# Performance work log

Measured on AMD Instinct MI355X. Metric: run time of the kernel, lower is better.

Reference implementation:

```python
import jax, jax.numpy as jnp
import numpy as np

H, O, E, V = 128, 128, 512, 34
B, T, L = 64, 2048, 256


def _lstm(x, wih, whh, bih, bhh):
    # x: [T, B, Din] -> outputs [T, B, H]; PyTorch gate order i, f, g, o
    n = whh.shape[1]
    h0 = jnp.zeros((x.shape[1], n), x.dtype)
    b = bih + bhh
    def step(carry, xt):
        h, c = carry
        g = xt @ wih.T + h @ whh.T + b
        i, f, gg, o = jnp.split(g, 4, axis=-1)
        c = jax.nn.sigmoid(f) * c + jax.nn.sigmoid(i) * jnp.tanh(gg)
        h = jax.nn.sigmoid(o) * jnp.tanh(c)
        return (h, c), h
    _, ys = jax.lax.scan(step, (h0, h0), x)
    return ys


def _conv1d_s2(x, w, b):
    # x: [B, Cin, T], w: [Cout, Cin, 2], kernel=2 stride=2 valid
    y = jax.lax.conv_general_dilated(x, w, (2,), 'VALID', dimension_numbers=('NCH', 'OIH', 'NCH'))
    return y + b[None, :, None]


def setup_inputs():
    key = jax.random.key(0)
    ctr = [0]
    def mk(shape, s=0.05):
        ctr[0] += 1
        return jax.random.normal(jax.random.fold_in(key, ctr[0]), shape, dtype=jnp.float32) * s
    inp = {}
    inp['utter'] = mk((B, T, 40), 1.0)
    inp['targets'] = jax.random.randint(jax.random.fold_in(key, 999), (B, L), 0, V)
    inp['wih_f'] = mk((4 * H, 40)); inp['whh_f'] = mk((4 * H, H)); inp['bih_f'] = mk((4 * H,)); inp['bhh_f'] = mk((4 * H,))
    inp['wih_r'] = mk((4 * H, 40)); inp['whh_r'] = mk((4 * H, H)); inp['bih_r'] = mk((4 * H,)); inp['bhh_r'] = mk((4 * H,))
    inp['c1w'] = mk((H, 2 * H, 2)); inp['c1b'] = mk((H,))
    inp['wih1'] = mk((4 * H, H)); inp['whh1'] = mk((4 * H, H)); inp['bih1'] = mk((4 * H,)); inp['bhh1'] = mk((4 * H,))
    inp['c2w'] = mk((H, H, 2)); inp['c2b'] = mk((H,))
    inp['wih2'] = mk((4 * H, H)); inp['whh2'] = mk((4 * H, H)); inp['bih2'] = mk((4 * H,)); inp['bhh2'] = mk((4 * H,))
    inp['kw'] = mk((O, H)); inp['kb'] = mk((O,)); inp['vw'] = mk((O, H)); inp['vb'] = mk((O,))
    inp['wihd'] = mk((4 * O, O + E)); inp['whhd'] = mk((4 * O, O)); inp['bihd'] = mk((4 * O,)); inp['bhhd'] = mk((4 * O,))
    inp['w1'] = mk((V, O)); inp['b1'] = mk((V,)); inp['w2'] = mk((V, O)); inp['b2'] = mk((V,))
    inp['w3'] = mk((V, V)); inp['b3'] = mk((V,))
    inp['emb'] = mk((V, E), 1.0)
    inp['sh0'] = mk((B, O)); inp['sc0'] = mk((B, O))
    return inp


def _forward(utter, targets, wih_f, whh_f, bih_f, bhh_f, wih_r, whh_r, bih_r, bhh_r,
             c1w, c1b, wih1, whh1, bih1, bhh1, c2w, c2b, wih2, whh2, bih2, bhh2,
             kw, kb, vw, vb, wihd, whhd, bihd, bhhd, w1, b1, w2, b2, w3, b3,
             emb, sh0, sc0):
    # ---- Listener (encoder) ----
    x = jnp.transpose(utter, (1, 0, 2))            # [T, B, 40]
    fwd = _lstm(x, wih_f, whh_f, bih_f, bhh_f)
    bwd = _lstm(x[::-1], wih_r, whh_r, bih_r, bhh_r)[::-1]
    h = jnp.concatenate([fwd, bwd], axis=-1)       # [T, B, 2H]
    h = jnp.transpose(h, (1, 2, 0))                # [B, 2H, T]
    h = _conv1d_s2(h, c1w, c1b)                    # [B, H, T/2]
    h = jnp.transpose(h, (2, 0, 1))                # [T/2, B, H]
    h = _lstm(h, wih1, whh1, bih1, bhh1)
    h = jnp.transpose(h, (1, 2, 0))
    h = _conv1d_s2(h, c2w, c2b)                    # [B, H, T/4]
    h = jnp.transpose(h, (2, 0, 1))
    h = _lstm(h, wih2, whh2, bih2, bhh2)
    h = jnp.transpose(h, (1, 0, 2))                # [B, T/4, H]
    hk = h @ kw.T + kb                              # [B, T/4, O]
    hv = h @ vw.T + vb
    # ---- Speller (decoder) ----
    ys = jnp.transpose(emb[targets], (1, 0, 2))[:-1]   # [L-1, B, E]
    mask = jnp.ones((utter.shape[0], hk.shape[1]), utter.dtype)  # all full-length
    bd = bihd + bhhd
    def step(carry, y_in):
        c, sh, sc = carry
        g = jnp.concatenate([y_in, c], axis=1) @ wihd.T + sh @ whhd.T + bd
        i, f, gg, o = jnp.split(g, 4, axis=-1)
        sc_n = jax.nn.sigmoid(f) * sc + jax.nn.sigmoid(i) * jnp.tanh(gg)
        sh_n = jax.nn.sigmoid(o) * jnp.tanh(sc_n)
        # NOTE: original attends with the cell state sc (faithful to source)
        att = jax.nn.softmax(jnp.einsum('btd,bd->bt', hk, sc_n), axis=1) * mask
        att = att / jnp.sum(att, axis=1, keepdims=True)
        c_n = jnp.einsum('bt,btd->bd', att, hv)
        out = jax.nn.relu(sh_n @ w1.T + b1 + c_n @ w2.T + b2)
        out = jax.nn.softmax(out @ w3.T + b3, axis=1)
        return (c_n, sh_n, sc_n), out
    c0 = jnp.zeros_like(sh0)
    _, preds = jax.lax.scan(step, (c0, sh0, sc0), ys)
    return jnp.transpose(preds, (1, 0, 2))         # [B, L-1, V]


def reference(utter, targets, wih_f, whh_f, bih_f, bhh_f, wih_r, whh_r, bih_r, bhh_r,
              c1w, c1b, wih1, whh1, bih1, bhh1, c2w, c2b, wih2, whh2, bih2, bhh2,
              kw, kb, vw, vb, wihd, whhd, bihd, bhhd, w1, b1, w2, b2, w3, b3,
              emb, sh0, sc0):
    return _forward(utter, targets, wih_f, whh_f, bih_f, bhh_f, wih_r, whh_r, bih_r, bhh_r,
                    c1w, c1b, wih1, whh1, bih1, bhh1, c2w, c2b, wih2, whh2, bih2, bhh2,
                    kw, kb, vw, vb, wihd, whhd, bihd, bhhd, w1, b1, w2, b2, w3, b3,
                    emb, sh0, sc0)
```

## Files before the change

### kernel.cpp

```cpp
#include <hip/hip_runtime.h>

typedef _Float16 half_t;
typedef _Float16 __attribute__((ext_vector_type(2))) half2_t;

__device__ __forceinline__ float fdot2_(half2_t a, half2_t b, float c) {
#if __has_builtin(__builtin_amdgcn_fdot2)
    return __builtin_amdgcn_fdot2(a, b, c, false);
#else
    return c + (float)a[0] * (float)b[0] + (float)a[1] * (float)b[1];
#endif
}
__device__ __forceinline__ half2_t h2(float a, float b) {
    half2_t r; r[0] = (half_t)a; r[1] = (half_t)b; return r;
}
__device__ __forceinline__ half2_t bc2(unsigned int u) {
    return __builtin_bit_cast(half2_t, u);
}
__device__ __forceinline__ unsigned int pk2(float a, float b) {
    return __builtin_bit_cast(unsigned int, h2(a, b));
}
__device__ __forceinline__ float sigm(float x) { return 1.0f / (1.0f + __expf(-x)); }
__device__ __forceinline__ float tanh_(float x) { return 1.0f - 2.0f / (1.0f + __expf(2.0f * x)); }
__device__ __forceinline__ unsigned int packbf2(float a, float b) {
    unsigned int ua = __float_as_uint(a);
    ua = (ua + 0x7fffu + ((ua >> 16) & 1u)) >> 16;
    unsigned int ub = __float_as_uint(b);
    ub = (ub + 0x7fffu + ((ub >> 16) & 1u)) >> 16;
    return ua | (ub << 16);
}
__device__ __forceinline__ float blo(unsigned int u) { return __uint_as_float(u << 16); }
__device__ __forceinline__ float bhi(unsigned int u) { return __uint_as_float(u & 0xffff0000u); }

#define ATTRS1024 __attribute__((amdgpu_flat_work_group_size(1024, 1024)))

__global__ __launch_bounds__(512, 1) void lstm1_k(
    const float* __restrict__ utter,
    const float* __restrict__ wih_f, const float* __restrict__ whh_f,
    const float* __restrict__ bih_f, const float* __restrict__ bhh_f,
    const float* __restrict__ wih_r, const float* __restrict__ whh_r,
    const float* __restrict__ bih_r, const float* __restrict__ bhh_r,
    unsigned short* __restrict__ Hf, unsigned short* __restrict__ Hr)
{
    const int tid = threadIdx.x;
    const int b   = blockIdx.x & 63;
    const int dir = blockIdx.x >> 6;
    const float* wih = dir ? wih_r : wih_f;
    const float* whh = dir ? whh_r : whh_f;
    const float* bih = dir ? bih_r : bih_f;
    const float* bhh = dir ? bhh_r : bhh_f;
    unsigned short* Hout = dir ? Hr : Hf;

    __shared__ float gates[512];
    __shared__ __align__(16) half_t h_h[128];
    __shared__ __align__(16) half_t x2[3][48];

    const int j = tid;
    unsigned int wr2[64];
    {
        const float4* wp = reinterpret_cast<const float4*>(whh + j * 128);
#pragma unroll
        for (int m = 0; m < 32; ++m) {
            float4 v = wp[m];
            wr2[2 * m]     = pk2(v.x, v.y);
            wr2[2 * m + 1] = pk2(v.z, v.w);
        }
    }
    unsigned int wx2[20];
    {
        const float4* xp = reinterpret_cast<const float4*>(wih + j * 40);
#pragma unroll
        for (int q = 0; q < 10; ++q) {
            float4 v = xp[q];
            wx2[2 * q]     = pk2(v.x, v.y);
            wx2[2 * q + 1] = pk2(v.z, v.w);
        }
    }
    const float bias = bih[j] + bhh[j];
    float c = 0.0f;
    if (tid < 128) h_h[tid] = (half_t)0.0f;
    if (tid < 40) {
        int tt0 = dir ? 2047 : 0;
        x2[0][tid] = (half_t)utter[((size_t)b * 2048 + tt0) * 40 + tid];
    } else if (tid < 80) {
        int tt1 = dir ? 2046 : 1;
        x2[1][tid - 40] = (half_t)utter[((size_t)b * 2048 + tt1) * 40 + (tid - 40)];
    }
    __syncthreads();

    for (int t = 0; t < 2048; ++t) {
        const int cur = t % 3;
        const int nx2 = (t + 2) % 3;
        float xn = 0.0f;
        const int tq = tid - 128;
        if (tq >= 0 && tq < 40) {
            int tn = (t + 2 < 2048) ? (t + 2) : 2047;
            int ttn = dir ? (2047 - tn) : tn;
            xn = utter[((size_t)b * 2048 + ttn) * 40 + tq];
        }
        float g0 = bias, g1 = 0.f, g2 = 0.f, g3 = 0.f;
        {
            const uint4* x4p = reinterpret_cast<const uint4*>(&x2[cur][0]);
#pragma unroll
            for (int q = 0; q < 5; ++q) {
                uint4 u = x4p[q];
                g0 = fdot2_(bc2(wx2[4 * q]),     bc2(u.x), g0);
                g1 = fdot2_(bc2(wx2[4 * q + 1]), bc2(u.y), g1);
                g2 = fdot2_(bc2(wx2[4 * q + 2]), bc2(u.z), g2);
                g3 = fdot2_(bc2(wx2[4 * q + 3]), bc2(u.w), g3);
            }
            const uint4* h4p = reinterpret_cast<const uint4*>(h_h);
#pragma unroll
            for (int q = 0; q < 16; ++q) {
                uint4 u = h4p[q];
                g0 = fdot2_(bc2(wr2[4 * q]),     bc2(u.x), g0);
                g1 = fdot2_(bc2(wr2[4 * q + 1]), bc2(u.y), g1);
                g2 = fdot2_(bc2(wr2[4 * q + 2]), bc2(u.z), g2);
                g3 = fdot2_(bc2(wr2[4 * q + 3]), bc2(u.w), g3);
            }
        }
        gates[j] = (g0 + g1) + (g2 + g3);
        __syncthreads();
        if (tid < 128) {
            float i_ = sigm(gates[tid]);
            float f_ = sigm(gates[128 + tid]);
            float g_ = tanh_(gates[256 + tid]);
            float o_ = sigm(gates[384 + tid]);
            c = f_ * c + i_ * g_;
            float hh = o_ * tanh_(c);
            half_t hx = (half_t)hh;
            h_h[tid] = hx;
            int tt = dir ? (2047 - t) : t;
            Hout[((size_t)tt * 64 + b) * 128 + tid] = __builtin_bit_cast(unsigned short, hx);
        } else if (tq < 40) {
            x2[nx2][tq] = (half_t)xn;
        }
        __syncthreads();
    }
}

__global__ __launch_bounds__(512, 1) void lstm_k(
    const unsigned short* __restrict__ Ph,
    const float* __restrict__ whh,
    void* __restrict__ Hout, int T, int outHalf)
{
    const int tid = threadIdx.x;
    const int b = blockIdx.x;
    const int j = tid;
    __shared__ float gates[512];
    __shared__ __align__(16) half_t h_h[128];
    unsigned int wr2[64];
    {
        const float4* wp = reinterpret_cast<const float4*>(whh + j * 128);
#pragma unroll
        for (int m = 0; m < 32; ++m) {
            float4 v = wp[m];
            wr2[2 * m]     = pk2(v.x, v.y);
            wr2[2 * m + 1] = pk2(v.z, v.w);
        }
    }
    float c = 0.0f;
    if (tid < 128) h_h[tid] = (half_t)0.0f;
    const size_t pbase = (size_t)b * T;
    float p_cur = (float)__builtin_bit_cast(half_t, Ph[(pbase + 0) * 512 + j]);
    float p_n1  = (float)__builtin_bit_cast(half_t, Ph[(pbase + 1) * 512 + j]);
    __syncthreads();
    for (int t = 0; t < T; ++t) {
        int tn = (t + 2 < T) ? (t + 2) : (T - 1);
        float p_n2 = (float)__builtin_bit_cast(half_t, Ph[(pbase + tn) * 512 + j]);
        float g0 = p_cur, g1 = 0.f, g2 = 0.f, g3 = 0.f;
        const uint4* h4p = reinterpret_cast<const uint4*>(h_h);
#pragma unroll
        for (int q = 0; q < 16; ++q) {
            uint4 u = h4p[q];
            g0 = fdot2_(bc2(wr2[4 * q]),     bc2(u.x), g0);
            g1 = fdot2_(bc2(wr2[4 * q + 1]), bc2(u.y), g1);
            g2 = fdot2_(bc2(wr2[4 * q + 2]), bc2(u.z), g2);
            g3 = fdot2_(bc2(wr2[4 * q + 3]), bc2(u.w), g3);
        }
        gates[j] = (g0 + g1) + (g2 + g3);
        __syncthreads();
        if (tid < 128) {
            float i_ = sigm(gates[tid]);
            float f_ = sigm(gates[128 + tid]);
            float g_ = tanh_(gates[256 + tid]);
            float o_ = sigm(gates[384 + tid]);
            c = f_ * c + i_ * g_;
            float hh = o_ * tanh_(c);
            half_t hx = (half_t)hh;
            h_h[tid] = hx;
            size_t oi = ((size_t)t * 64 + b) * 128 + tid;
            if (outHalf) ((unsigned short*)Hout)[oi] = __builtin_bit_cast(unsigned short, hx);
            else         ((float*)Hout)[oi] = hh;
        }
        __syncthreads();
        p_cur = p_n1;
        p_n1 = p_n2;
    }
}

template <int CIN>
__global__ __launch_bounds__(128) void conv_k(
    const unsigned short* __restrict__ HA, const unsigned short* __restrict__ HB,
    const float* __restrict__ W, const float* __restrict__ bias,
    float* __restrict__ out, int Tout)
{
    __shared__ __align__(16) float xin[64 * CIN];
    const int b = blockIdx.x;
    const int t0 = blockIdx.y * 32;
    const int tid = threadIdx.x;
    for (int idx = tid; idx < 64 * CIN; idx += 128) {
        int tl = idx / CIN, ci = idx % CIN;
        int tau = t0 * 2 + tl;
        unsigned short u;
        if constexpr (CIN == 256) {
            u = (ci < 128) ? HA[(size_t)tau * 8192 + b * 128 + ci]
                           : HB[(size_t)tau * 8192 + b * 128 + (ci - 128)];
        } else {
            u = HA[(size_t)tau * 8192 + b * 128 + ci];
        }
        xin[idx] = (float)__builtin_bit_cast(half_t, u);
    }
    __syncthreads();
    const int co = tid;
    float acc[32];
#pragma unroll
    for (int u = 0; u < 32; ++u) acc[u] = 0.0f;
    const float4* Wrow4 = reinterpret_cast<const float4*>(W + (size_t)co * 2 * CIN);
    const float4* xin4 = reinterpret_cast<const float4*>(xin);
    for (int c4 = 0; c4 < CIN / 4; ++c4) {
        float4 wA = Wrow4[2 * c4];
        float4 wB = Wrow4[2 * c4 + 1];
#pragma unroll
        for (int u = 0; u < 32; ++u) {
            float4 x0 = xin4[(2 * u) * (CIN / 4) + c4];
            float4 x1 = xin4[(2 * u + 1) * (CIN / 4) + c4];
            acc[u] += wA.x * x0.x + wA.y * x1.x + wA.z * x0.y + wA.w * x1.y
                    + wB.x * x0.z + wB.y * x1.z + wB.z * x0.w + wB.w * x1.w;
        }
    }
    float bs = bias[co];
#pragma unroll
    for (int u = 0; u < 32; ++u)
        out[((size_t)b * Tout + t0 + u) * 128 + co] = acc[u] + bs;
}

__global__ __launch_bounds__(256) void gemm_k(
    const float* __restrict__ A, const float* __restrict__ W, int ldw,
    const float* __restrict__ bias1, const float* __restrict__ bias2,
    void* __restrict__ C, int M, int N, int K, int mode, int Tdim)
{
    __shared__ __align__(16) float As[16][68];
    __shared__ __align__(16) float Ws[16][68];
    const int tid = threadIdx.x;
    const int m0 = blockIdx.x * 64, n0 = blockIdx.y * 64;
    const int kk = tid & 15, mm = tid >> 4;
    const int tm = tid & 15, tn = tid >> 4;
    float acc[4][4];
#pragma unroll
    for (int i = 0; i < 4; ++i)
#pragma unroll
        for (int jj = 0; jj < 4; ++jj) acc[i][jj] = 0.0f;

    for (int k0 = 0; k0 < K; k0 += 16) {
#pragma unroll
        for (int r = 0; r < 4; ++r) {
            As[kk][mm + 16 * r] = A[(size_t)(m0 + mm + 16 * r) * K + k0 + kk];
            Ws[kk][mm + 16 * r] = W[(size_t)(n0 + mm + 16 * r) * ldw + k0 + kk];
        }
        __syncthreads();
#pragma unroll
        for (int q = 0; q < 16; ++q) {
            float4 a = reinterpret_cast<const float4*>(&As[q][0])[tm];
            float4 w = reinterpret_cast<const float4*>(&Ws[q][0])[tn];
            acc[0][0] += a.x * w.x; acc[0][1] += a.x * w.y; acc[0][2] += a.x * w.z; acc[0][3] += a.x * w.w;
            acc[1][0] += a.y * w.x; acc[1][1] += a.y * w.y; acc[1][2] += a.y * w.z; acc[1][3] += a.y * w.w;
            acc[2][0] += a.z * w.x; acc[2][1] += a.z * w.y; acc[2][2] += a.z * w.z; acc[2][3] += a.z * w.w;
            acc[3][0] += a.w * w.x; acc[3][1] += a.w * w.y; acc[3][2] += a.w * w.z; acc[3][3] += a.w * w.w;
        }
        __syncthreads();
    }
    float bv[4];
#pragma unroll
    for (int jj = 0; jj < 4; ++jj) {
        int n = n0 + tn * 4 + jj;
        float v = 0.0f;
        if (bias1) v += bias1[n];
        if (bias2) v += bias2[n];
        bv[jj] = v;
    }
#pragma unroll
    for (int i = 0; i < 4; ++i) {
        int m = m0 + tm * 4 + i;
#pragma unroll
        for (int jj = 0; jj < 4; ++jj) {
            int n = n0 + tn * 4 + jj;
            float v = acc[i][jj] + bv[jj];
            if (mode == 0) {
                ((float*)C)[(size_t)m * N + n] = v;
            } else if (mode == 1) {
                int bb = m & 63, tt = m >> 6;
                ((float*)C)[((size_t)bb * N + n) * Tdim + tt] = v;
            } else {
                ((unsigned short*)C)[(size_t)m * N + n] =
                    __builtin_bit_cast(unsigned short, (half_t)v);
            }
        }
    }
}

__global__ __launch_bounds__(512) void packemb_k(
    const int* __restrict__ targets, const float* __restrict__ emb,
    float* __restrict__ Ypack)
{
    int m = blockIdx.x;
    int l = m >> 6, b = m & 63;
    int tgt = targets[b * 256 + l];
    Ypack[(size_t)m * 512 + threadIdx.x] = emb[(size_t)tgt * 512 + threadIdx.x];
}

__global__ __launch_bounds__(256) void packq_k(
    const float* __restrict__ src, unsigned int* __restrict__ dst,
    int srcCols, int colOff, int nq, int rows)
{
    int g = blockIdx.x * 256 + threadIdx.x;
    if (g >= rows * nq * 4) return;
    int k = g & 3, t = g >> 2;
    int j = t % rows, q = t / rows;
    int p = q * 4 + k;
    const float* s = src + (size_t)j * srcCols + colOff + 2 * p;
    dst[g] = pk2(s[0], s[1]);
}

__global__ __launch_bounds__(1024) void packhv2_k(
    const float* __restrict__ hvT, unsigned int* __restrict__ hvq)
{
    int b = blockIdx.x;
    for (int it = 0; it < 32; ++it) {
        int idx = it * 1024 + threadIdx.x;
        int tq = idx >> 7, d = idx & 127;
        const float* s = hvT + ((size_t)b * 128 + d) * 512 + 2 * tq;
        hvq[(size_t)b * 32768 + idx] = packbf2(s[0], s[1]);
    }
}

__global__ ATTRS1024 void decoder_k(
    const float* __restrict__ Yp,
    const unsigned int* __restrict__ Wd,
    const float* __restrict__ hk,
    const unsigned int* __restrict__ hvq,
    const float* __restrict__ sh0, const float* __restrict__ sc0,
    float* __restrict__ SHs, float* __restrict__ Cs)
{
    __shared__ unsigned int hk_lds[512][66];
    __shared__ float pflat[1024];
    __shared__ __align__(16) half_t sh_h[128];
    __shared__ __align__(16) float sc_f[128];
    __shared__ __align__(16) half_t c_h[128];
    __shared__ __align__(16) float att[512];
    __shared__ float red[8];

    const int tid = threadIdx.x;
    const int b = blockIdx.x;
    const int role = tid >> 9;
    const int j = tid & 511;

    const uint4* Wd4 = reinterpret_cast<const uint4*>(Wd) + (size_t)role * 8192;

    {
        const float4* hp = reinterpret_cast<const float4*>(hk + ((size_t)j * 64 + b) * 128 + role * 64);
#pragma unroll
        for (int q = 0; q < 16; ++q) {
            float4 v = hp[q];
            hk_lds[j][role * 32 + 2 * q]     = packbf2(v.x, v.y);
            hk_lds[j][role * 32 + 2 * q + 1] = packbf2(v.z, v.w);
        }
    }
    float sc_r = 0.0f;
    if (tid < 128) {
        sh_h[tid] = (half_t)sh0[b * 128 + tid];
        sc_r = sc0[b * 128 + tid];
        sc_f[tid] = sc_r;
        c_h[tid] = (half_t)0.0f;
    }
    __syncthreads();

    const int wid = tid >> 6, lane = tid & 63;
    const int g8 = tid >> 7, d = tid & 127;
    const unsigned int* hvp = hvq + (size_t)b * 32768 + g8 * 32 * 128 + d;
    const float2* att2 = reinterpret_cast<const float2*>(att);
    float yp_cur = (role == 0) ? Yp[(size_t)b * 512 + j] : 0.0f;

    for (int l = 0; l < 255; ++l) {
        int lnxt = (l + 1 < 255) ? (l + 1) : l;
        float yp_nxt = (role == 0) ? Yp[((size_t)lnxt * 64 + b) * 512 + j] : 0.0f;
        {
            float g0 = yp_cur, g1 = 0.f, g2 = 0.f, g3 = 0.f;
            const uint4* s4 = reinterpret_cast<const uint4*>(role ? c_h : sh_h);
#pragma unroll
            for (int q = 0; q < 16; ++q) {
                uint4 w = Wd4[q * 512 + j];
                uint4 u = s4[q];
                g0 = fdot2_(bc2(w.x), bc2(u.x), g0);
                g1 = fdot2_(bc2(w.y), bc2(u.y), g1);
                g2 = fdot2_(bc2(w.z), bc2(u.z), g2);
                g3 = fdot2_(bc2(w.w), bc2(u.w), g3);
            }
            pflat[tid] = (g0 + g1) + (g2 + g3);
        }
        __syncthreads();
        if (tid < 128) {
            float i_ = sigm(pflat[tid]       + pflat[512 + tid]);
            float f_ = sigm(pflat[128 + tid] + pflat[640 + tid]);
            float g_ = tanh_(pflat[256 + tid] + pflat[768 + tid]);
            float o_ = sigm(pflat[384 + tid] + pflat[896 + tid]);
            sc_r = f_ * sc_r + i_ * g_;
            float hh = o_ * tanh_(sc_r);
            sh_h[tid] = (half_t)hh;
            sc_f[tid] = sc_r;
            SHs[((size_t)l * 64 + b) * 128 + tid] = hh;
        }
        __syncthreads();
        if (tid < 512) {
            float e0 = 0.f, e1 = 0.f, e2 = 0.f, e3 = 0.f;
            const uint2* hkr = reinterpret_cast<const uint2*>(&hk_lds[tid][0]);
            const float4* sc4 = reinterpret_cast<const float4*>(sc_f);
#pragma unroll
            for (int q = 0; q < 32; ++q) {
                uint2 u = hkr[q];
                float4 s = sc4[q];
                e0 += blo(u.x) * s.x; e1 += bhi(u.x) * s.y;
                e2 += blo(u.y) * s.z; e3 += bhi(u.y) * s.w;
            }
            float p = __expf((e0 + e1) + (e2 + e3));
            att[tid] = p;
            float ps = p;
#pragma unroll
            for (int off = 32; off; off >>= 1) ps += __shfl_xor(ps, off);
            if (lane == 0) red[wid] = ps;
        }
        __syncthreads();
        {
            float a0 = 0.f, a1 = 0.f;
#pragma unroll
            for (int i = 0; i < 32; i += 2) {
                unsigned int u0 = hvp[(size_t)i * 128];
                unsigned int u1 = hvp[(size_t)(i + 1) * 128];
                float2 w0 = att2[g8 * 32 + i];
                float2 w1 = att2[g8 * 32 + i + 1];
                a0 += blo(u0) * w0.x + bhi(u0) * w0.y;
                a1 += blo(u1) * w1.x + bhi(u1) * w1.y;
            }
            pflat[tid] = a0 + a1;
        }
        __syncthreads();
        if (tid < 128) {
            float S = ((red[0] + red[1]) + (red[2] + red[3]))
                    + ((red[4] + red[5]) + (red[6] + red[7]));
            float cs = 0.f;
#pragma unroll
            for (int g = 0; g < 8; ++g) cs += pflat[g * 128 + tid];
            float cv = cs / S;
            c_h[tid] = (half_t)cv;
            Cs[((size_t)l * 64 + b) * 128 + tid] = cv;
        }
        yp_cur = yp_nxt;
        __syncthreads();
    }
}

__global__ __launch_bounds__(256) void mlp_k(
    const float* __restrict__ SHs, const float* __restrict__ Cs,
    const float* __restrict__ w1, const float* __restrict__ b1,
    const float* __restrict__ w2, const float* __restrict__ b2,
    const float* __restrict__ w3, const float* __restrict__ b3,
    float* __restrict__ out)
{
    __shared__ float o_l[4][34];
    const int sub = threadIdx.x >> 6, lane = threadIdx.x & 63;
    const int m = blockIdx.x * 4 + sub;
    const int l = m >> 6, b = m & 63;
    if (lane < 34) {
        float o1 = b1[lane] + b2[lane];
        const float4* w1r = reinterpret_cast<const float4*>(w1 + lane * 128);
        const float4* w2r = reinterpret_cast<const float4*>(w2 + lane * 128);
        const float4* sh4 = reinterpret_cast<const float4*>(SHs + (size_t)m * 128);
        const float4* c4  = reinterpret_cast<const float4*>(Cs + (size_t)m * 128);
#pragma unroll 8
        for (int q = 0; q < 32; ++q) {
            float4 a = w1r[q], h = sh4[q], w = w2r[q], cc = c4[q];
            o1 += a.x * h.x + a.y * h.y + a.z * h.z + a.w * h.w
                + w.x * cc.x + w.y * cc.y + w.z * cc.z + w.w * cc.w;
        }
        o_l[sub][lane] = fmaxf(o1, 0.0f);
    }
    __syncthreads();
    if (lane < 34) {
        float zz = b3[lane];
        const float* w3r = w3 + lane * 34;
        for (int v = 0; v < 34; ++v) zz += w3r[v] * o_l[sub][v];
        __syncthreads();
        o_l[sub][lane] = zz;
        __syncthreads();
        float zm = o_l[sub][0];
        for (int v = 1; v < 34; ++v) zm = fmaxf(zm, o_l[sub][v]);
        float Ssum = 0.0f;
        for (int v = 0; v < 34; ++v) Ssum += __expf(o_l[sub][v] - zm);
        out[((size_t)b * 255 + l) * 34 + lane] = __expf(zz - zm) / Ssum;
    }
}

extern "C" void kernel_launch(void* const* d_in, const int* in_sizes, int n_in,
                              void* d_out, int out_size, void* d_ws, size_t ws_size,
                              hipStream_t stream) {
    (void)in_sizes; (void)n_in; (void)out_size; (void)ws_size;
    const float* utter = (const float*)d_in[0];
    const int*   targets = (const int*)d_in[1];
    const float* wih_f = (const float*)d_in[2];
    const float* whh_f = (const float*)d_in[3];
    const float* bih_f = (const float*)d_in[4];
    const float* bhh_f = (const float*)d_in[5];
    const float* wih_r = (const float*)d_in[6];
    const float* whh_r = (const float*)d_in[7];
    const float* bih_r = (const float*)d_in[8];
    const float* bhh_r = (const float*)d_in[9];
    const float* c1w = (const float*)d_in[10];
    const float* c1b = (const float*)d_in[11];
    const float* wih1 = (const float*)d_in[12];
    const float* whh1 = (const float*)d_in[13];
    const float* bih1 = (const float*)d_in[14];
    const float* bhh1 = (const float*)d_in[15];
    const float* c2w = (const float*)d_in[16];
    const float* c2b = (const float*)d_in[17];
    const float* wih2 = (const float*)d_in[18];
    const float* whh2 = (const float*)d_in[19];
    const float* bih2 = (const float*)d_in[20];
    const float* bhh2 = (const float*)d_in[21];
    const float* kw = (const float*)d_in[22];
    const float* kb = (const float*)d_in[23];
    const float* vw = (const float*)d_in[24];
    const float* vb = (const float*)d_in[25];
    const float* wihd = (const float*)d_in[26];
    const float* whhd = (const float*)d_in[27];
    const float* bihd = (const float*)d_in[28];
    const float* bhhd = (const float*)d_in[29];
    const float* w1 = (const float*)d_in[30];
    const float* b1 = (const float*)d_in[31];
    const float* w2 = (const float*)d_in[32];
    const float* b2 = (const float*)d_in[33];
    const float* w3 = (const float*)d_in[34];
    const float* b3 = (const float*)d_in[35];
    const float* emb = (const float*)d_in[36];
    const float* sh0 = (const float*)d_in[37];
    const float* sc0 = (const float*)d_in[38];

    char* ws = (char*)d_ws;
    const size_t MB = 1ull << 20;
    unsigned int* Wd = (unsigned int*)(ws + 0);

    unsigned short* Hf_h   = (unsigned short*)(ws + 1 * MB);
    unsigned short* Hr_h   = (unsigned short*)(ws + 33 * MB);
    float*          conv1o = (float*)(ws + 65 * MB);
    unsigned short* P2_h   = (unsigned short*)(ws + 1 * MB);
    unsigned short* H2_h   = (unsigned short*)(ws + 65 * MB);
    float*          conv2o = (float*)(ws + 81 * MB);
    unsigned short* P3_h   = (unsigned short*)(ws + 97 * MB);
    float*          H3     = (float*)(ws + 1 * MB);
    float*          hkb    = (float*)(ws + 17 * MB);
    float*          hvT    = (float*)(ws + 33 * MB);
    unsigned int*   hvq    = (unsigned int*)(ws + 49 * MB);
    float*          Ypack  = (float*)(ws + 57 * MB);
    float*          Yp     = (float*)(ws + 89 * MB);
    float*          SHsave = (float*)(ws + 121 * MB);
    float*          Csave  = (float*)(ws + 130 * MB);

    packq_k<<<128, 256, 0, stream>>>(whhd, Wd + 0,     128, 0,   16, 512);
    packq_k<<<128, 256, 0, stream>>>(wihd, Wd + 32768, 640, 512, 16, 512);

    lstm1_k<<<128, 512, 0, stream>>>(utter, wih_f, whh_f, bih_f, bhh_f,
                                     wih_r, whh_r, bih_r, bhh_r, Hf_h, Hr_h);
    conv_k<256><<<dim3(64, 32), 128, 0, stream>>>(Hf_h, Hr_h, c1w, c1b, conv1o, 1024);
    gemm_k<<<dim3(1024, 8), 256, 0, stream>>>(conv1o, wih1, 128, bih1, bhh1,
                                              P2_h, 65536, 512, 128, 2, 0);
    lstm_k<<<64, 512, 0, stream>>>(P2_h, whh1, H2_h, 1024, 1);
    conv_k<128><<<dim3(64, 16), 128, 0, stream>>>(H2_h, nullptr, c2w, c2b, conv2o, 512);
    gemm_k<<<dim3(512, 8), 256, 0, stream>>>(conv2o, wih2, 128, bih2, bhh2,
                                             P3_h, 32768, 512, 128, 2, 0);
    lstm_k<<<64, 512, 0, stream>>>(P3_h, whh2, H3, 512, 0);
    gemm_k<<<dim3(512, 2), 256, 0, stream>>>(H3, kw, 128, kb, nullptr,
                                             hkb, 32768, 128, 128, 0, 0);
    gemm_k<<<dim3(512, 2), 256, 0, stream>>>(H3, vw, 128, vb, nullptr,
                                             hvT, 32768, 128, 128, 1, 512);
    packhv2_k<<<64, 1024, 0, stream>>>(hvT, hvq);
    packemb_k<<<16320, 512, 0, stream>>>(targets, emb, Ypack);
    gemm_k<<<dim3(255, 8), 256, 0, stream>>>(Ypack, wihd, 640, bihd, bhhd,
                                             Yp, 16320, 512, 512, 0, 0);
    decoder_k<<<64, 1024, 0, stream>>>(Yp, Wd, hkb, hvq, sh0, sc0, SHsave, Csave);
    mlp_k<<<4080, 256, 0, stream>>>(SHsave, Csave, w1, b1, w2, b2, w3, b3, (float*)d_out);
}
```

Measured before the change: 5.932 ms.

## Spread LSTM gate activations across all threads and shrink decoder to 512 threads

```diff
diff --git a/kernel.cpp b/kernel.cpp
--- a/kernel.cpp
+++ b/kernel.cpp
@@ -31,8 +31,6 @@
 __device__ __forceinline__ float blo(unsigned int u) { return __uint_as_float(u << 16); }
 __device__ __forceinline__ float bhi(unsigned int u) { return __uint_as_float(u & 0xffff0000u); }
 
-#define ATTRS1024 __attribute__((amdgpu_flat_work_group_size(1024, 1024)))
-
 __global__ __launch_bounds__(512, 1) void lstm1_k(
     const float* __restrict__ utter,
     const float* __restrict__ wih_f, const float* __restrict__ whh_f,
@@ -50,11 +48,12 @@
     const float* bhh = dir ? bhh_r : bhh_f;
     unsigned short* Hout = dir ? Hr : Hf;
 
-    __shared__ float gates[512];
+    __shared__ float acts[512];
     __shared__ __align__(16) half_t h_h[128];
     __shared__ __align__(16) half_t x2[3][48];
 
     const int j = tid;
+    const int gt = tid >> 7;
     unsigned int wr2[64];
     {
         const float4* wp = reinterpret_cast<const float4*>(whh + j * 128);
@@ -118,13 +117,14 @@
                 g3 = fdot2_(bc2(wr2[4 * q + 3]), bc2(u.w), g3);
             }
         }
-        gates[j] = (g0 + g1) + (g2 + g3);
+        float g = (g0 + g1) + (g2 + g3);
+        acts[j] = (gt == 2) ? tanh_(g) : sigm(g);
         __syncthreads();
         if (tid < 128) {
-            float i_ = sigm(gates[tid]);
-            float f_ = sigm(gates[128 + tid]);
-            float g_ = tanh_(gates[256 + tid]);
-            float o_ = sigm(gates[384 + tid]);
+            float i_ = acts[tid];
+            float f_ = acts[128 + tid];
+            float g_ = acts[256 + tid];
+            float o_ = acts[384 + tid];
             c = f_ * c + i_ * g_;
             float hh = o_ * tanh_(c);
             half_t hx = (half_t)hh;
@@ -146,7 +146,8 @@
     const int tid = threadIdx.x;
     const int b = blockIdx.x;
     const int j = tid;
-    __shared__ float gates[512];
+    const int gt = tid >> 7;
+    __shared__ float acts[512];
     __shared__ __align__(16) half_t h_h[128];
     unsigned int wr2[64];
     {
@@ -177,13 +178,14 @@
             g2 = fdot2_(bc2(wr2[4 * q + 2]), bc2(u.z), g2);
             g3 = fdot2_(bc2(wr2[4 * q + 3]), bc2(u.w), g3);
         }
-        gates[j] = (g0 + g1) + (g2 + g3);
+        float g = (g0 + g1) + (g2 + g3);
+        acts[j] = (gt == 2) ? tanh_(g) : sigm(g);
         __syncthreads();
         if (tid < 128) {
-            float i_ = sigm(gates[tid]);
-            float f_ = sigm(gates[128 + tid]);
-            float g_ = tanh_(gates[256 + tid]);
-            float o_ = sigm(gates[384 + tid]);
+            float i_ = acts[tid];
+            float f_ = acts[128 + tid];
+            float g_ = acts[256 + tid];
+            float o_ = acts[384 + tid];
             c = f_ * c + i_ * g_;
             float hh = o_ * tanh_(c);
             half_t hx = (half_t)hh;
@@ -343,7 +345,7 @@
     }
 }
 
-__global__ ATTRS1024 void decoder_k(
+__global__ __launch_bounds__(512, 1) void decoder_k(
     const float* __restrict__ Yp,
     const unsigned int* __restrict__ Wd,
     const float* __restrict__ hk,
@@ -352,7 +354,8 @@
     float* __restrict__ SHs, float* __restrict__ Cs)
 {
     __shared__ unsigned int hk_lds[512][66];
-    __shared__ float pflat[1024];
+    __shared__ float acts[512];
+    __shared__ float pfl[512];
     __shared__ __align__(16) half_t sh_h[128];
     __shared__ __align__(16) float sc_f[128];
     __shared__ __align__(16) half_t c_h[128];
@@ -361,18 +364,23 @@
 
     const int tid = threadIdx.x;
     const int b = blockIdx.x;
-    const int role = tid >> 9;
-    const int j = tid & 511;
-
-    const uint4* Wd4 = reinterpret_cast<const uint4*>(Wd) + (size_t)role * 8192;
-
+    const int gt = tid >> 7;
+
+    uint4 wh[16];
     {
-        const float4* hp = reinterpret_cast<const float4*>(hk + ((size_t)j * 64 + b) * 128 + role * 64);
-#pragma unroll
-        for (int q = 0; q < 16; ++q) {
+        const uint4* W4 = reinterpret_cast<const uint4*>(Wd);
+#pragma unroll
+        for (int q = 0; q < 16; ++q) wh[q] = W4[q * 512 + tid];
+    }
+    const uint4* Wc4 = reinterpret_cast<const uint4*>(Wd) + 8192;
+
+    {
+        const float4* hp = reinterpret_cast<const float4*>(hk + ((size_t)tid * 64 + b) * 128);
+#pragma unroll
+        for (int q = 0; q < 32; ++q) {
             float4 v = hp[q];
-            hk_lds[j][role * 32 + 2 * q]     = packbf2(v.x, v.y);
-            hk_lds[j][role * 32 + 2 * q + 1] = packbf2(v.z, v.w);
+            hk_lds[tid][2 * q]     = packbf2(v.x, v.y);
+            hk_lds[tid][2 * q + 1] = packbf2(v.z, v.w);
         }
     }
     float sc_r = 0.0f;
@@ -385,34 +393,44 @@
     __syncthreads();
 
     const int wid = tid >> 6, lane = tid & 63;
-    const int g8 = tid >> 7, d = tid & 127;
-    const unsigned int* hvp = hvq + (size_t)b * 32768 + g8 * 32 * 128 + d;
+    const int g4 = tid >> 7, d = tid & 127;
+    const unsigned int* hvp = hvq + (size_t)b * 32768 + (size_t)(g4 * 64) * 128 + d;
     const float2* att2 = reinterpret_cast<const float2*>(att);
-    float yp_cur = (role == 0) ? Yp[(size_t)b * 512 + j] : 0.0f;
+    float yp_cur = Yp[(size_t)b * 512 + tid];
 
     for (int l = 0; l < 255; ++l) {
         int lnxt = (l + 1 < 255) ? (l + 1) : l;
-        float yp_nxt = (role == 0) ? Yp[((size_t)lnxt * 64 + b) * 512 + j] : 0.0f;
+        float yp_nxt = Yp[((size_t)lnxt * 64 + b) * 512 + tid];
         {
             float g0 = yp_cur, g1 = 0.f, g2 = 0.f, g3 = 0.f;
-            const uint4* s4 = reinterpret_cast<const uint4*>(role ? c_h : sh_h);
+            const uint4* s4 = reinterpret_cast<const uint4*>(sh_h);
 #pragma unroll
             for (int q = 0; q < 16; ++q) {
-                uint4 w = Wd4[q * 512 + j];
                 uint4 u = s4[q];
+                g0 = fdot2_(bc2(wh[q].x), bc2(u.x), g0);
+                g1 = fdot2_(bc2(wh[q].y), bc2(u.y), g1);
+                g2 = fdot2_(bc2(wh[q].z), bc2(u.z), g2);
+                g3 = fdot2_(bc2(wh[q].w), bc2(u.w), g3);
+            }
+            const uint4* c4 = reinterpret_cast<const uint4*>(c_h);
+#pragma unroll
+            for (int q = 0; q < 16; ++q) {
+                uint4 w = Wc4[q * 512 + tid];
+                uint4 u = c4[q];
                 g0 = fdot2_(bc2(w.x), bc2(u.x), g0);
                 g1 = fdot2_(bc2(w.y), bc2(u.y), g1);
                 g2 = fdot2_(bc2(w.z), bc2(u.z), g2);
                 g3 = fdot2_(bc2(w.w), bc2(u.w), g3);
             }
-            pflat[tid] = (g0 + g1) + (g2 + g3);
+            float g = (g0 + g1) + (g2 + g3);
+            acts[tid] = (gt == 2) ? tanh_(g) : sigm(g);
         }
         __syncthreads();
         if (tid < 128) {
-            float i_ = sigm(pflat[tid]       + pflat[512 + tid]);
-            float f_ = sigm(pflat[128 + tid] + pflat[640 + tid]);
-            float g_ = tanh_(pflat[256 + tid] + pflat[768 + tid]);
-            float o_ = sigm(pflat[384 + tid] + pflat[896 + tid]);
+            float i_ = acts[tid];
+            float f_ = acts[128 + tid];
+            float g_ = acts[256 + tid];
+            float o_ = acts[384 + tid];
             sc_r = f_ * sc_r + i_ * g_;
             float hh = o_ * tanh_(sc_r);
             sh_h[tid] = (half_t)hh;
@@ -420,7 +438,7 @@
             SHs[((size_t)l * 64 + b) * 128 + tid] = hh;
         }
         __syncthreads();
-        if (tid < 512) {
+        {
             float e0 = 0.f, e1 = 0.f, e2 = 0.f, e3 = 0.f;
             const uint2* hkr = reinterpret_cast<const uint2*>(&hk_lds[tid][0]);
             const float4* sc4 = reinterpret_cast<const float4*>(sc_f);
@@ -441,25 +459,22 @@
         __syncthreads();
         {
             float a0 = 0.f, a1 = 0.f;
-#pragma unroll
-            for (int i = 0; i < 32; i += 2) {
+#pragma unroll 8
+            for (int i = 0; i < 64; i += 2) {
                 unsigned int u0 = hvp[(size_t)i * 128];
                 unsigned int u1 = hvp[(size_t)(i + 1) * 128];
-                float2 w0 = att2[g8 * 32 + i];
-                float2 w1 = att2[g8 * 32 + i + 1];
+                float2 w0 = att2[g4 * 64 + i];
+                float2 w1 = att2[g4 * 64 + i + 1];
                 a0 += blo(u0) * w0.x + bhi(u0) * w0.y;
                 a1 += blo(u1) * w1.x + bhi(u1) * w1.y;
             }
-            pflat[tid] = a0 + a1;
+            pfl[tid] = a0 + a1;
         }
         __syncthreads();
         if (tid < 128) {
             float S = ((red[0] + red[1]) + (red[2] + red[3]))
                     + ((red[4] + red[5]) + (red[6] + red[7]));
-            float cs = 0.f;
-#pragma unroll
-            for (int g = 0; g < 8; ++g) cs += pflat[g * 128 + tid];
-            float cv = cs / S;
+            float cv = (pfl[tid] + pfl[128 + tid] + pfl[256 + tid] + pfl[384 + tid]) / S;
             c_h[tid] = (half_t)cv;
             Cs[((size_t)l * 64 + b) * 128 + tid] = cv;
         }
@@ -594,6 +609,6 @@
     packemb_k<<<16320, 512, 0, stream>>>(targets, emb, Ypack);
     gemm_k<<<dim3(255, 8), 256, 0, stream>>>(Ypack, wihd, 640, bihd, bhhd,
                                              Yp, 16320, 512, 512, 0, 0);
-    decoder_k<<<64, 1024, 0, stream>>>(Yp, Wd, hkb, hvq, sh0, sc0, SHsave, Csave);
+    decoder_k<<<64, 512, 0, stream>>>(Yp, Wd, hkb, hvq, sh0, sc0, SHsave, Csave);
     mlp_k<<<4080, 256, 0, stream>>>(SHsave, Csave, w1, b1, w2, b2, w3, b3, (float*)d_out);
 }
```

After: 5.353 ms. 1.11x faster.
